# Optimization experiments

Hardware: AMD Instinct MI355X
Metric: run time of the kernel (lower is better)

The kernel has to match this reference:

```python
import jax, jax.numpy as jnp
import numpy as np

LRELU_SLOPE = 0.2
ACT_GAIN = np.float32(np.sqrt(2.0))  # bias_act lrelu gain in StyleGAN2


def _per_sample_conv3x3(x, w):
    """Grouped-conv-as-batch trick: per-sample 3x3 conv.
    x: [B, C, H, W], w: [B, O, C, 3, 3] -> [B, O, H, W] (padding=1)."""
    def one(xi, wi):
        return jax.lax.conv_general_dilated(
            xi[None], wi, window_strides=(1, 1), padding=[(1, 1), (1, 1)],
            dimension_numbers=('NCHW', 'OIHW', 'NCHW'))[0]
    return jax.vmap(one)(x, w)


def setup_inputs() -> dict:
    key = jax.random.key(0)
    ks = jax.random.split(key, 10)
    B, C, R, W_DIM, IMG_C = 16, 512, 64, 512, 3
    inv_sqrt_c = np.float32(1.0 / np.sqrt(W_DIM))
    return {
        'ws': jax.random.normal(ks[0], (B, 2, W_DIM), jnp.float32),
        'const': jax.random.normal(ks[1], (C, R, R), jnp.float32),
        'conv_w': jax.random.normal(ks[2], (C, C, 3, 3), jnp.float32),
        'conv_b': jnp.zeros((C,), jnp.float32),
        'conv_aff_w': jax.random.normal(ks[3], (C, W_DIM), jnp.float32) * inv_sqrt_c,
        'conv_aff_b': jnp.ones((C,), jnp.float32),
        'noise_const': jax.random.normal(ks[4], (R, R), jnp.float32),
        'noise_strength': jnp.full((1,), 0.1, jnp.float32),
        'rgb_w': jax.random.normal(ks[5], (IMG_C, C, 1, 1), jnp.float32),
        'rgb_b': jnp.zeros((IMG_C,), jnp.float32),
        'rgb_aff_w': jax.random.normal(ks[6], (C, W_DIM), jnp.float32) * inv_sqrt_c,
        'rgb_aff_b': jnp.ones((C,), jnp.float32),
    }


def reference(ws, const, conv_w, conv_b, conv_aff_w, conv_aff_b,
              noise_const, noise_strength, rgb_w, rgb_b, rgb_aff_w, rgb_aff_b):
    B = ws.shape[0]
    # const input broadcast to batch (in_channels == 0 block)
    x = jnp.broadcast_to(const[None], (B,) + const.shape)

    # --- SynthesisLayer: modulated_conv2d (demodulate=True, fused_modconv=True) ---
    s = ws[:, 0] @ conv_aff_w.T + conv_aff_b                    # [B, C] styles
    w = conv_w[None] * s[:, None, :, None, None]                # [B, O, C, 3, 3] modulate
    dcoefs = jax.lax.rsqrt(jnp.sum(jnp.square(w), axis=(2, 3, 4)) + 1e-8)  # [B, O]
    w = w * dcoefs[:, :, None, None, None]                      # demodulate
    x = _per_sample_conv3x3(x, w)                               # grouped conv trick
    x = x + noise_const[None, None] * noise_strength            # fused noise add
    x = jax.nn.leaky_relu(x + conv_b[None, :, None, None], LRELU_SLOPE) * ACT_GAIN

    # --- ToRGBLayer: modulated 1x1 conv, demodulate=False ---
    weight_gain = np.float32(1.0 / np.sqrt(conv_w.shape[1]))    # 1/sqrt(in_ch*kh*kw)
    s2 = (ws[:, 1] @ rgb_aff_w.T + rgb_aff_b) * weight_gain     # [B, C]
    img = jnp.einsum('bchw,oc,bc->bohw', x, rgb_w[:, :, 0, 0], s2)
    img = img + rgb_b[None, :, None, None]
    return x, img
```

## Files before the change

kernel.cpp:

```cpp
#include <hip/hip_runtime.h>
#include <hip/hip_bf16.h>

typedef __attribute__((ext_vector_type(8))) short short8;
typedef __attribute__((ext_vector_type(4))) float f32x4;
typedef __attribute__((ext_vector_type(16))) float f32x16;

#define LRELU_SLOPE 0.2f
#define ACT_GAIN 1.41421356237309515f
#define WG_RGB 0.04419417382415922f

__device__ __forceinline__ void glds16(const short* g, short* l) {
    __builtin_amdgcn_global_load_lds(
        (const __attribute__((address_space(1))) unsigned int*)g,
        (__attribute__((address_space(3))) unsigned int*)l, 16, 0, 0);
}

__global__ void k_init(__hip_bfloat16* __restrict__ Ypad,
                       const float* __restrict__ rgb_b, float* __restrict__ img) {
    int blk = blockIdx.x, tid = threadIdx.x;
    if (blk < 1040) {
        int gslot = blk*4 + (tid >> 6);
        int b = gslot / 260;
        int cell = gslot - b*260;
        int h, w;
        if (cell < 66)       { h = 0;          w = cell; }
        else if (cell < 132) { h = 65;         w = cell - 66; }
        else if (cell < 196) { h = cell - 131; w = 0; }
        else                 { h = cell - 195; w = 65; }
        short8 z = {};
        *(short8*)((short*)Ypad + (((b*66 + h)*66) + w)*512 + (tid & 63)*8) = z;
    } else {
        int blk2 = blk - 1040;
        #pragma unroll
        for (int j = 0; j < 4; ++j) {
            int f4 = blk2*1024 + j*256 + tid;
            int b3 = f4 >> 10;
            int o3 = b3 % 3;
            float v = rgb_b[o3];
            f32x4 vv = {v, v, v, v};
            *(f32x4*)(img + f4*4) = vv;
        }
    }
}

__global__ void k_styles(const float* __restrict__ wsin,
                         const float* __restrict__ caw, const float* __restrict__ cab,
                         const float* __restrict__ raw_, const float* __restrict__ rab,
                         float* __restrict__ sbuf, float* __restrict__ s2buf) {
    int b = blockIdx.x, which = blockIdx.y;
    int tid = threadIdx.x, lane = tid & 63, wv = tid >> 6;
    const float* aw = which ? raw_ : caw;
    const float* ab = which ? rab : cab;
    float scale = which ? WG_RGB : 1.0f;
    float* op = which ? s2buf : sbuf;
    __shared__ float wsv[512];
    wsv[tid]       = wsin[(b*2 + which)*512 + tid];
    wsv[tid + 256] = wsin[(b*2 + which)*512 + tid + 256];
    __syncthreads();
    for (int c = wv; c < 512; c += 4) {
        float p = 0.f;
        #pragma unroll
        for (int kk = 0; kk < 8; ++kk)
            p += aw[c*512 + kk*64 + lane] * wsv[kk*64 + lane];
        #pragma unroll
        for (int off = 32; off; off >>= 1) p += __shfl_down(p, off, 64);
        if (lane == 0) op[b*512 + c] = (p + ab[c]) * scale;
    }
}

__global__ __launch_bounds__(256) void k_prepw(const float* __restrict__ conv_w,
                        float* __restrict__ w2sum, __hip_bfloat16* __restrict__ Abf) {
    int o = blockIdx.x, tid = threadIdx.x;
    __shared__ float wrow[4608];
    const f32x4* src = (const f32x4*)(conv_w + o*4608);
    #pragma unroll
    for (int r = 0; r < 5; ++r) {
        int idx = tid + (r << 8);
        if (idx < 1152) *(f32x4*)&wrow[idx*4] = src[idx];
    }
    __syncthreads();
    #pragma unroll
    for (int j = 0; j < 2; ++j) {
        int c = tid + (j << 8);
        float sum = 0.f;
        #pragma unroll
        for (int t = 0; t < 9; ++t) {
            float v = wrow[c*9 + t];
            sum += v*v;
            Abf[(t*512 + o)*512 + c] = __float2bfloat16(v);
        }
        w2sum[o*512 + c] = sum;
    }
}

__global__ __launch_bounds__(256) void k_dcoef(const float* __restrict__ sbuf,
                                               const float* __restrict__ w2sum,
                                               const float* __restrict__ s2buf,
                                               const float* __restrict__ rgb_w,
                                               float* __restrict__ dcoef,
                                               float* __restrict__ rgbc) {
    int gw = blockIdx.x*4 + (threadIdx.x >> 6);
    int lane = threadIdx.x & 63;
    int b = gw >> 9, o = gw & 511;
    float acc = 0.f;
    #pragma unroll
    for (int i = 0; i < 8; ++i) {
        int c = (i << 6) + lane;
        float sv = sbuf[(b << 9) + c];
        acc += sv*sv*w2sum[(o << 9) + c];
    }
    #pragma unroll
    for (int off = 32; off; off >>= 1) acc += __shfl_down(acc, off, 64);
    if (lane == 0) dcoef[(b << 9) + o] = rsqrtf(acc + 1e-8f);
    if (blockIdx.x < 96) {
        int flat = blockIdx.x*256 + threadIdx.x;
        int bb = flat / 1536;
        int r  = flat - bb*1536;
        int c  = r & 511;
        rgbc[flat] = rgb_w[r] * s2buf[bb*512 + c];
    }
}

__global__ void k_ypad(const float* __restrict__ cst, const float* __restrict__ sbuf,
                       __hip_bfloat16* __restrict__ Ypad) {
    int b = blockIdx.x >> 6, h = blockIdx.x & 63, tid = threadIdx.x;
    __shared__ float tile[64][65];
    for (int cc = 0; cc < 8; ++cc) {
        int c0 = cc << 6;
        #pragma unroll
        for (int it = 0; it < 16; ++it) {
            int cl = (it << 2) + (tid >> 6);
            int w = tid & 63;
            tile[cl][w] = cst[(c0 + cl)*4096 + (h << 6) + w];
        }
        __syncthreads();
        #pragma unroll
        for (int it = 0; it < 16; ++it) {
            int flat = (it << 8) + tid;
            int w = flat >> 6, cl = flat & 63;
            float v = sbuf[(b << 9) + c0 + cl] * tile[cl][w];
            Ypad[(((b*66 + h + 1)*66) + (w + 1))*512 + c0 + cl] = __float2bfloat16(v);
        }
        __syncthreads();
    }
}

__global__ __launch_bounds__(256, 2) void conv_gemm(
    const short* __restrict__ Abf,
    const short* __restrict__ Ypad,
    const float* __restrict__ dcoef,
    const float* __restrict__ noise,
    const float* __restrict__ nstr,
    const float* __restrict__ bias,
    const float* __restrict__ rgbc,
    float* __restrict__ xout,
    float* __restrict__ img)
{
    __shared__ short SH[22528];
    short* Aring = SH;
    short* Bbuf  = SH + 16384;
    float (*red)[3][2] = (float (*)[3][2])SH;

    int tid = threadIdx.x, lane = tid & 63, wv = tid >> 6;
    int wr = wv >> 1, wc = wv & 1;
    int ml32 = lane & 31, hi = lane >> 5;

    int blk = blockIdx.x;
    int xcd = blk & 7, idx = blk >> 3;
    int v = xcd * 128 + idx;
    int mblk = v & 1, nblk = v >> 1;
    int b = nblk >> 5;
    int n0 = (nblk & 31) << 7;
    int h0 = n0 >> 6;
    int o0 = mblk << 8;

    int bgofs[3];
    #pragma unroll
    for (int r = 0; r < 3; ++r) {
        int s = tid + (r << 8);
        int pos = s >> 1; if (pos > 263) pos = 263;
        int q = (s & 1) ^ (((pos >> 2) ^ (pos >> 3)) & 1);
        int hl = pos / 66, ww = pos - hl * 66;
        bgofs[r] = (((b*66 + h0 + hl)*66) + ww)*512 + q*8;
    }
    int agofs[2];
    #pragma unroll
    for (int r = 0; r < 2; ++r) {
        int s = tid + (r << 8);
        int row = s >> 1;
        int q = (s & 1) ^ (((row >> 2) ^ (row >> 3)) & 1);
        agofs[r] = ((o0 + row) << 9) + q*8;
    }
    int aro[4];
    #pragma unroll
    for (int mi = 0; mi < 4; ++mi) {
        int row = wr*128 + mi*32 + ml32;
        aro[mi] = row*16 + ((hi ^ (((row >> 2) ^ (row >> 3)) & 1)) << 3);
    }
    int pb0 = wc*66 + ml32;

    short* AW = Aring + wv*512;
    short* BW = Bbuf + wv*512;

    f32x16 acc[4][2] = {};
    short8 fa[2][4], fb[2][2];

    #pragma unroll
    for (int t = 0; t < 3; ++t) {
        glds16(Abf + (t << 18) + agofs[0], AW + t*4096);
        glds16(Abf + (t << 18) + agofs[1], AW + t*4096 + 2048);
    }
    asm volatile("s_waitcnt vmcnt(0)" ::: "memory");
    __builtin_amdgcn_s_barrier();

#define FRAGRD(SET, SLOT, TAPX)                                             \
    { _Pragma("unroll")                                                     \
      for (int mi = 0; mi < 4; ++mi)                                        \
          fa[SET][mi] = *(const short8*)(Aring + (SLOT)*4096 + aro[mi]);    \
      _Pragma("unroll")                                                     \
      for (int ni = 0; ni < 2; ++ni) {                                      \
          int p_ = pb0 + ((TAPX)/3)*66 + ((TAPX)%3) + ni*32;                \
          int jx = (hi ^ (((p_ >> 2) ^ (p_ >> 3)) & 1)) << 3;               \
          fb[SET][ni] = *(const short8*)(Bbuf + p_*16 + jx); } }

#define MMCL(SET)                                                           \
    __builtin_amdgcn_s_setprio(1);                                          \
    _Pragma("unroll")                                                       \
    for (int mi = 0; mi < 4; ++mi)                                          \
        _Pragma("unroll")                                                   \
        for (int ni = 0; ni < 2; ++ni)                                      \
            acc[mi][ni] = __builtin_amdgcn_mfma_f32_32x32x16_bf16(          \
                fa[SET][mi], fb[SET][ni], acc[mi][ni], 0, 0, 0);            \
    __builtin_amdgcn_s_setprio(0);

#define PHASE(TAP, CUR, C0, C0N, RB)                                        \
    {                                                                       \
        int rr  = ((RB) + (TAP)) & 3;                                       \
        int rrN = ((RB) + (TAP) + 1) & 3;                                   \
        int rw  = ((RB) + (TAP) + 3) & 3;                                   \
        constexpr int TAPN = ((TAP) + 1) % 9;                               \
        constexpr int TAPP = ((TAP) < 6) ? (TAP) + 3 : (TAP) - 6;           \
        constexpr int NXT = (CUR) ^ 1;                                      \
        if ((TAP) == 0) {                                                   \
            glds16(Ypad + bgofs[0] + (C0), BW);                             \
            glds16(Ypad + bgofs[1] + (C0), BW + 2048);                      \
            glds16(Ypad + bgofs[2] + (C0), BW + 4096);                      \
        }                                                                   \
        { const short* asrc_ = Abf + (TAPP << 18) + (((TAP) < 6) ? (C0) : (C0N)); \
          glds16(asrc_ + agofs[0], AW + rw*4096);                           \
          glds16(asrc_ + agofs[1], AW + rw*4096 + 2048); }                  \
        if ((TAP) == 0) {                                                   \
            asm volatile("s_waitcnt vmcnt(2)" ::: "memory");                \
            __builtin_amdgcn_s_barrier();                                   \
            FRAGRD(CUR, rr, 0)                                              \
        }                                                                   \
        if ((TAP) < 8) { FRAGRD(NXT, rrN, TAPN) }                           \
        __builtin_amdgcn_sched_barrier(0);                                  \
        MMCL(CUR)                                                           \
        asm volatile("s_waitcnt vmcnt(2)" ::: "memory");                    \
        __builtin_amdgcn_s_barrier();                                       \
    }

#define CHUNK9(PAR, C0, C0N, RB)                                            \
    PHASE(0, ((0+(PAR))&1), C0, C0N, RB) PHASE(1, ((1+(PAR))&1), C0, C0N, RB) \
    PHASE(2, ((2+(PAR))&1), C0, C0N, RB) PHASE(3, ((3+(PAR))&1), C0, C0N, RB) \
    PHASE(4, ((4+(PAR))&1), C0, C0N, RB) PHASE(5, ((5+(PAR))&1), C0, C0N, RB) \
    PHASE(6, ((6+(PAR))&1), C0, C0N, RB) PHASE(7, ((7+(PAR))&1), C0, C0N, RB) \
    PHASE(8, ((8+(PAR))&1), C0, C0N, RB)

    for (int cc = 0; cc < 16; ++cc) {
        int c0e = cc << 5;
        int rbe = (cc << 1) & 3;
        CHUNK9(0, c0e, c0e + 16, rbe)
        int c0o = c0e + 16;
        int c0no = (c0e + 32) & 511;
        CHUNK9(1, c0o, c0no, (rbe + 1) & 3)
    }
#undef PHASE
#undef CHUNK9
#undef FRAGRD
#undef MMCL

    asm volatile("s_waitcnt vmcnt(0)" ::: "memory");
    __builtin_amdgcn_s_barrier();

    float ns = nstr[0];
    float pr0[2] = {0.f, 0.f}, pr1[2] = {0.f, 0.f}, pr2[2] = {0.f, 0.f};
    #pragma unroll
    for (int mi = 0; mi < 4; ++mi) {
        int ob = o0 + wr*128 + mi*32 + hi*4;
        f32x4 dc[4], bs[4], c0r[4], c1r[4], c2r[4];
        #pragma unroll
        for (int g = 0; g < 4; ++g) {
            dc[g]  = *(const f32x4*)(dcoef + (b << 9) + ob + g*8);
            bs[g]  = *(const f32x4*)(bias + ob + g*8);
            c0r[g] = *(const f32x4*)(rgbc + b*1536 + ob + g*8);
            c1r[g] = *(const f32x4*)(rgbc + b*1536 + 512 + ob + g*8);
            c2r[g] = *(const f32x4*)(rgbc + b*1536 + 1024 + ob + g*8);
        }
        #pragma unroll
        for (int ni = 0; ni < 2; ++ni) {
            int nl = wc*64 + ni*32 + ml32;
            int hw = n0 + nl;
            float nz = noise[hw] * ns;
            #pragma unroll
            for (int g = 0; g < 4; ++g)
                #pragma unroll
                for (int t = 0; t < 4; ++t) {
                    float vv = acc[mi][ni][g*4 + t] * dc[g][t] + nz + bs[g][t];
                    vv = (vv < 0.f ? LRELU_SLOPE*vv : vv) * ACT_GAIN;
                    xout[(((b << 9) + ob + g*8 + t) << 12) + hw] = vv;
                    pr0[ni] += vv * c0r[g][t];
                    pr1[ni] += vv * c1r[g][t];
                    pr2[ni] += vv * c2r[g][t];
                }
        }
    }
    #pragma unroll
    for (int ni = 0; ni < 2; ++ni) {
        pr0[ni] += __shfl_down(pr0[ni], 32, 64);
        pr1[ni] += __shfl_down(pr1[ni], 32, 64);
        pr2[ni] += __shfl_down(pr2[ni], 32, 64);
    }
    if (lane < 32) {
        #pragma unroll
        for (int ni = 0; ni < 2; ++ni) {
            int nl = wc*64 + ni*32 + ml32;
            red[nl][0][wr] = pr0[ni];
            red[nl][1][wr] = pr1[ni];
            red[nl][2][wr] = pr2[ni];
        }
    }
    __syncthreads();
    for (int p = tid; p < 384; p += 256) {
        int o3 = p >> 7, nl = p & 127;
        atomicAdd(img + ((b*3 + o3) << 12) + n0 + nl, red[nl][o3][0] + red[nl][o3][1]);
    }
}

extern "C" void kernel_launch(void* const* d_in, const int* in_sizes, int n_in,
                              void* d_out, int out_size, void* d_ws, size_t ws_size,
                              hipStream_t stream) {
    (void)in_sizes; (void)n_in; (void)out_size; (void)ws_size;
    const float* wsin   = (const float*)d_in[0];
    const float* cst    = (const float*)d_in[1];
    const float* conv_w = (const float*)d_in[2];
    const float* conv_b = (const float*)d_in[3];
    const float* caw    = (const float*)d_in[4];
    const float* cab    = (const float*)d_in[5];
    const float* noise  = (const float*)d_in[6];
    const float* nstr   = (const float*)d_in[7];
    const float* rgb_w  = (const float*)d_in[8];
    const float* rgb_b  = (const float*)d_in[9];
    const float* raw_   = (const float*)d_in[10];
    const float* rab    = (const float*)d_in[11];

    char* wsb = (char*)d_ws;
    float* sbuf   = (float*)(wsb + 0);
    float* s2buf  = (float*)(wsb + 32768);
    float* dcoef  = (float*)(wsb + 65536);
    float* rgbc   = (float*)(wsb + 98304);
    float* w2sum  = (float*)(wsb + 196608);
    __hip_bfloat16* Abf  = (__hip_bfloat16*)(wsb + 1245184);
    __hip_bfloat16* Ypad = (__hip_bfloat16*)(wsb + 5963776);

    float* xout = (float*)d_out;
    float* img  = xout + 33554432;

    k_init<<<1088, 256, 0, stream>>>(Ypad, rgb_b, img);
    k_styles<<<dim3(16, 2), 256, 0, stream>>>(wsin, caw, cab, raw_, rab, sbuf, s2buf);
    k_prepw<<<512, 256, 0, stream>>>(conv_w, w2sum, Abf);
    k_dcoef<<<2048, 256, 0, stream>>>(sbuf, w2sum, s2buf, rgb_w, dcoef, rgbc);
    k_ypad<<<1024, 256, 0, stream>>>(cst, sbuf, Ypad);
    conv_gemm<<<1024, 256, 0, stream>>>((const short*)Abf, (const short*)Ypad,
                                        dcoef, noise, nstr, conv_b, rgbc, xout, img);
}
```

Measured before the change: 667.7 us.

## Enlarge conv GEMM tile to 256x256 with 512 threads and K=32 chunks

Each conv_gemm block now covers 256 output channels by 256 pixels using 8 waves, up from 128 pixels and 4 waves, and the grid is halved. Each chunk now spans 32 input channels split into two K=16 halves, and the B halo tile is double-buffered so the next chunk's input rows prefetch during the current 9 taps. The aim is to raise reuse of the A weight tile, amortise barriers, and overlap B loads with MFMA work. In exchange LDS use grows to about 116KB per block and register pressure rises, which may limit occupancy. The wait counts and barrier layout become more intricate and easier to get wrong.

```diff
diff --git a/kernel.cpp b/kernel.cpp
--- a/kernel.cpp
+++ b/kernel.cpp
@@ -8,6 +8,7 @@
 #define LRELU_SLOPE 0.2f
 #define ACT_GAIN 1.41421356237309515f
 #define WG_RGB 0.04419417382415922f
+#define X1(v) ((((v) >> 2) ^ ((v) >> 3)) & 1)
 
 __device__ __forceinline__ void glds16(const short* g, short* l) {
     __builtin_amdgcn_global_load_lds(
@@ -145,7 +146,7 @@
     }
 }
 
-__global__ __launch_bounds__(256, 2) void conv_gemm(
+__global__ __launch_bounds__(512, 2) void conv_gemm(
     const short* __restrict__ Abf,
     const short* __restrict__ Ypad,
     const float* __restrict__ dcoef,
@@ -156,129 +157,155 @@
     float* __restrict__ xout,
     float* __restrict__ img)
 {
-    __shared__ short SH[22528];
+    __shared__ short SH[59392];
     short* Aring = SH;
-    short* Bbuf  = SH + 16384;
+    short* Bbuf  = SH + 32768;
     float (*red)[3][2] = (float (*)[3][2])SH;
 
     int tid = threadIdx.x, lane = tid & 63, wv = tid >> 6;
-    int wr = wv >> 1, wc = wv & 1;
+    int wr = wv >> 2, wc = wv & 3;
     int ml32 = lane & 31, hi = lane >> 5;
 
     int blk = blockIdx.x;
     int xcd = blk & 7, idx = blk >> 3;
-    int v = xcd * 128 + idx;
+    int v = xcd * 64 + idx;
     int mblk = v & 1, nblk = v >> 1;
-    int b = nblk >> 5;
-    int n0 = (nblk & 31) << 7;
-    int h0 = n0 >> 6;
+    int b = nblk >> 4;
+    int hw0 = (nblk & 15) << 8;
+    int h0 = hw0 >> 6;
     int o0 = mblk << 8;
 
-    int bgofs[3];
+    int bsrc[3];
     #pragma unroll
     for (int r = 0; r < 3; ++r) {
-        int s = tid + (r << 8);
-        int pos = s >> 1; if (pos > 263) pos = 263;
-        int q = (s & 1) ^ (((pos >> 2) ^ (pos >> 3)) & 1);
-        int hl = pos / 66, ww = pos - hl * 66;
-        bgofs[r] = (((b*66 + h0 + hl)*66) + ww)*512 + q*8;
+        int j = tid + (r << 9);
+        int ks = (j >= 832) ? 1 : 0;
+        int pe = (j - ks*832) >> 1;
+        int pos = pe > 395 ? 395 : pe;
+        int half = j & 1;
+        int q = half ^ X1(pos);
+        int hl = pos / 66, ww = pos - hl*66;
+        bsrc[r] = (((b*66 + h0 + hl)*66) + ww)*512 + ks*16 + q*8;
+    }
+    int bsrc3;
+    {
+        int j = 1536 + wv*16 + (lane & 15);
+        int pe = (j - 832) >> 1;
+        int pos = pe > 395 ? 395 : pe;
+        int half = j & 1;
+        int q = half ^ X1(pos);
+        int hl = pos / 66, ww = pos - hl*66;
+        bsrc3 = (((b*66 + h0 + hl)*66) + ww)*512 + 16 + q*8;
     }
     int agofs[2];
     #pragma unroll
     for (int r = 0; r < 2; ++r) {
-        int s = tid + (r << 8);
-        int row = s >> 1;
-        int q = (s & 1) ^ (((row >> 2) ^ (row >> 3)) & 1);
-        agofs[r] = ((o0 + row) << 9) + q*8;
+        int row = tid >> 1, half = tid & 1;
+        int q = half ^ X1(row);
+        agofs[r] = ((o0 + row) << 9) + r*16 + q*8;
     }
     int aro[4];
     #pragma unroll
     for (int mi = 0; mi < 4; ++mi) {
         int row = wr*128 + mi*32 + ml32;
-        aro[mi] = row*16 + ((hi ^ (((row >> 2) ^ (row >> 3)) & 1)) << 3);
+        aro[mi] = row*16 + ((hi ^ X1(row)) << 3);
     }
     int pb0 = wc*66 + ml32;
+    const int BPA[9] = {0, 1, 2, 66, 67, 68, 132, 133, 134};
 
     short* AW = Aring + wv*512;
-    short* BW = Bbuf + wv*512;
 
     f32x16 acc[4][2] = {};
-    short8 fa[2][4], fb[2][2];
-
+    short8 faA[4], fbA[2], faB[4], fbB[2];
+
+    #pragma unroll
+    for (int r = 0; r < 3; ++r)
+        glds16(Ypad + bsrc[r], Bbuf + wv*512 + r*4096);
+    if ((lane & 63) < 16) glds16(Ypad + bsrc3, Bbuf + 12288 + wv*128);
     #pragma unroll
     for (int t = 0; t < 3; ++t) {
-        glds16(Abf + (t << 18) + agofs[0], AW + t*4096);
-        glds16(Abf + (t << 18) + agofs[1], AW + t*4096 + 2048);
-    }
-    asm volatile("s_waitcnt vmcnt(0)" ::: "memory");
+        glds16(Abf + (t << 18) + agofs[0], AW + t*8192);
+        glds16(Abf + (t << 18) + agofs[1], AW + t*8192 + 4096);
+    }
+    asm volatile("s_waitcnt vmcnt(2)" ::: "memory");
     __builtin_amdgcn_s_barrier();
-
-#define FRAGRD(SET, SLOT, TAPX)                                             \
-    { _Pragma("unroll")                                                     \
-      for (int mi = 0; mi < 4; ++mi)                                        \
-          fa[SET][mi] = *(const short8*)(Aring + (SLOT)*4096 + aro[mi]);    \
-      _Pragma("unroll")                                                     \
-      for (int ni = 0; ni < 2; ++ni) {                                      \
-          int p_ = pb0 + ((TAPX)/3)*66 + ((TAPX)%3) + ni*32;                \
-          int jx = (hi ^ (((p_ >> 2) ^ (p_ >> 3)) & 1)) << 3;               \
-          fb[SET][ni] = *(const short8*)(Bbuf + p_*16 + jx); } }
-
-#define MMCL(SET)                                                           \
+    #pragma unroll
+    for (int mi = 0; mi < 4; ++mi)
+        faA[mi] = *(const short8*)(Aring + aro[mi]);
+    #pragma unroll
+    for (int ni = 0; ni < 2; ++ni) {
+        int p_ = pb0 + ni*32;
+        fbA[ni] = *(const short8*)(Bbuf + p_*16 + ((hi ^ X1(p_)) << 3));
+    }
+
+    constexpr int VMP[9] = {3, 3, 3, 3, 2, 2, 2, 2, 2};
+
+#define MMCL(FA, FB)                                                        \
     __builtin_amdgcn_s_setprio(1);                                          \
     _Pragma("unroll")                                                       \
     for (int mi = 0; mi < 4; ++mi)                                          \
         _Pragma("unroll")                                                   \
         for (int ni = 0; ni < 2; ++ni)                                      \
             acc[mi][ni] = __builtin_amdgcn_mfma_f32_32x32x16_bf16(          \
-                fa[SET][mi], fb[SET][ni], acc[mi][ni], 0, 0, 0);            \
+                FA[mi], FB[ni], acc[mi][ni], 0, 0, 0);                      \
     __builtin_amdgcn_s_setprio(0);
 
-#define PHASE(TAP, CUR, C0, C0N, RB)                                        \
+#define PH(TAP)                                                             \
     {                                                                       \
-        int rr  = ((RB) + (TAP)) & 3;                                       \
-        int rrN = ((RB) + (TAP) + 1) & 3;                                   \
-        int rw  = ((RB) + (TAP) + 3) & 3;                                   \
+        int rr  = (rb + (TAP)) & 3;                                         \
+        int rrN = (rb + (TAP) + 1) & 3;                                     \
+        int rw  = (rb + (TAP) + 3) & 3;                                     \
         constexpr int TAPN = ((TAP) + 1) % 9;                               \
         constexpr int TAPP = ((TAP) < 6) ? (TAP) + 3 : (TAP) - 6;           \
-        constexpr int NXT = (CUR) ^ 1;                                      \
-        if ((TAP) == 0) {                                                   \
-            glds16(Ypad + bgofs[0] + (C0), BW);                             \
-            glds16(Ypad + bgofs[1] + (C0), BW + 2048);                      \
-            glds16(Ypad + bgofs[2] + (C0), BW + 4096);                      \
+                                            \
+        _Pragma("unroll")                                                   \
+        for (int mi = 0; mi < 4; ++mi)                                      \
+            faB[mi] = *(const short8*)(Aring + rr*8192 + 4096 + aro[mi]);   \
+        _Pragma("unroll")                                                   \
+        for (int ni = 0; ni < 2; ++ni) {                                    \
+            int p_ = pb0 + BPA[(TAP)] + ni*32;                              \
+            fbB[ni] = *(const short8*)(Bcur + 6656 + p_*16                  \
+                                       + ((hi ^ X1(p_)) << 3));             \
         }                                                                   \
-        { const short* asrc_ = Abf + (TAPP << 18) + (((TAP) < 6) ? (C0) : (C0N)); \
-          glds16(asrc_ + agofs[0], AW + rw*4096);                           \
-          glds16(asrc_ + agofs[1], AW + rw*4096 + 2048); }                  \
-        if ((TAP) == 0) {                                                   \
-            asm volatile("s_waitcnt vmcnt(2)" ::: "memory");                \
-            __builtin_amdgcn_s_barrier();                                   \
-            FRAGRD(CUR, rr, 0)                                              \
-        }                                                                   \
-        if ((TAP) < 8) { FRAGRD(NXT, rrN, TAPN) }                           \
+             \
+        { const short* asrc_ = Abf + (TAPP << 18) + (((TAP) < 6) ? c0 : c0n); \
+          glds16(asrc_ + agofs[0], AW + rw*8192);                           \
+          glds16(asrc_ + agofs[1], AW + rw*8192 + 4096); }                  \
+        if ((TAP) < 3) glds16(Ypad + bsrc[(TAP)] + c0n, BWn + (TAP)*4096);  \
+        if ((TAP) == 3) { if ((lane & 63) < 16)                             \
+            glds16(Ypad + bsrc3 + c0n, BRm); }                              \
         __builtin_amdgcn_sched_barrier(0);                                  \
-        MMCL(CUR)                                                           \
-        asm volatile("s_waitcnt vmcnt(2)" ::: "memory");                    \
+        MMCL(faA, fbA)                                                      \
+        __builtin_amdgcn_sched_barrier(0);                                  \
+                                                  \
+        { const short* BbN = ((TAP) == 8) ? Bnxt : Bcur;                    \
+          _Pragma("unroll")                                                 \
+          for (int mi = 0; mi < 4; ++mi)                                    \
+              faA[mi] = *(const short8*)(Aring + rrN*8192 + aro[mi]);       \
+          _Pragma("unroll")                                                 \
+          for (int ni = 0; ni < 2; ++ni) {                                  \
+              int p_ = pb0 + BPA[TAPN] + ni*32;                             \
+              fbA[ni] = *(const short8*)(BbN + p_*16                        \
+                                         + ((hi ^ X1(p_)) << 3));           \
+          } }                                                               \
+        __builtin_amdgcn_sched_barrier(0);                                  \
+        MMCL(faB, fbB)                                                      \
+        asm volatile("s_waitcnt vmcnt(%0)" :: "i"(VMP[(TAP)]) : "memory");  \
         __builtin_amdgcn_s_barrier();                                       \
     }
 
-#define CHUNK9(PAR, C0, C0N, RB)                                            \
-    PHASE(0, ((0+(PAR))&1), C0, C0N, RB) PHASE(1, ((1+(PAR))&1), C0, C0N, RB) \
-    PHASE(2, ((2+(PAR))&1), C0, C0N, RB) PHASE(3, ((3+(PAR))&1), C0, C0N, RB) \
-    PHASE(4, ((4+(PAR))&1), C0, C0N, RB) PHASE(5, ((5+(PAR))&1), C0, C0N, RB) \
-    PHASE(6, ((6+(PAR))&1), C0, C0N, RB) PHASE(7, ((7+(PAR))&1), C0, C0N, RB) \
-    PHASE(8, ((8+(PAR))&1), C0, C0N, RB)
-
-    for (int cc = 0; cc < 16; ++cc) {
-        int c0e = cc << 5;
-        int rbe = (cc << 1) & 3;
-        CHUNK9(0, c0e, c0e + 16, rbe)
-        int c0o = c0e + 16;
-        int c0no = (c0e + 32) & 511;
-        CHUNK9(1, c0o, c0no, (rbe + 1) & 3)
-    }
-#undef PHASE
-#undef CHUNK9
-#undef FRAGRD
+    for (int ch = 0; ch < 16; ++ch) {
+        int c0 = ch << 5;
+        int c0n = (c0 + 32) & 511;
+        int rb = ch & 3;
+        int half = ch & 1;
+        const short* Bcur = Bbuf + half*13312;
+        const short* Bnxt = Bbuf + (half ^ 1)*13312;
+        short* BWn = (short*)Bnxt + wv*512;
+        short* BRm = (short*)Bnxt + 12288 + wv*128;
+        PH(0) PH(1) PH(2) PH(3) PH(4) PH(5) PH(6) PH(7) PH(8)
+    }
+#undef PH
 #undef MMCL
 
     asm volatile("s_waitcnt vmcnt(0)" ::: "memory");
@@ -301,7 +328,7 @@
         #pragma unroll
         for (int ni = 0; ni < 2; ++ni) {
             int nl = wc*64 + ni*32 + ml32;
-            int hw = n0 + nl;
+            int hw = hw0 + nl;
             float nz = noise[hw] * ns;
             #pragma unroll
             for (int g = 0; g < 4; ++g)
@@ -332,9 +359,9 @@
         }
     }
     __syncthreads();
-    for (int p = tid; p < 384; p += 256) {
-        int o3 = p >> 7, nl = p & 127;
-        atomicAdd(img + ((b*3 + o3) << 12) + n0 + nl, red[nl][o3][0] + red[nl][o3][1]);
+    for (int p = tid; p < 768; p += 512) {
+        int o3 = p >> 8, nl = p & 255;
+        atomicAdd(img + ((b*3 + o3) << 12) + hw0 + nl, red[nl][o3][0] + red[nl][o3][1]);
     }
 }
 
@@ -372,6 +399,6 @@
     k_prepw<<<512, 256, 0, stream>>>(conv_w, w2sum, Abf);
     k_dcoef<<<2048, 256, 0, stream>>>(sbuf, w2sum, s2buf, rgb_w, dcoef, rgbc);
     k_ypad<<<1024, 256, 0, stream>>>(cst, sbuf, Ypad);
-    conv_gemm<<<1024, 256, 0, stream>>>((const short*)Abf, (const short*)Ypad,
-                                        dcoef, noise, nstr, conv_b, rgbc, xout, img);
-}
+    conv_gemm<<<512, 512, 0, stream>>>((const short*)Abf, (const short*)Ypad,
+                                       dcoef, noise, nstr, conv_b, rgbc, xout, img);
+}
```

Result: faster. 572.9 us (-14.2%).
